# Kernel tuning notes

Hardware: AMD Instinct MI355X
Metric: run time of the kernel (lower is better)

Reference implementation:

```python
import jax, jax.numpy as jnp
import numpy as np

NUM_CENTROIDS = 2048
EMA_DECAY = 0.99
GAMMA = 1.0
EPS = 1e-08


def setup_inputs() -> dict:
    key = jax.random.key(0)
    k1, k2 = jax.random.split(key)
    B, T, D = 32, 512, 512
    inputs = jax.random.normal(k1, (B, T, D), dtype=jnp.float32)
    # variance_scaling(0.1, 'fan_avg', 'normal') init for the codebook
    fan_avg = (NUM_CENTROIDS + D) / 2.0
    std = np.sqrt(0.1 / fan_avg).astype(np.float32)
    codebook = jax.random.normal(k2, (NUM_CENTROIDS, D), dtype=jnp.float32) * std
    cluster_counts = jnp.ones((NUM_CENTROIDS,), dtype=jnp.float32)
    return {"inputs": inputs, "codebook": codebook,
            "cluster_counts": cluster_counts, "train": 1}


def reference(inputs, codebook, cluster_counts, train):
    D = inputs.shape[-1]
    K = codebook.shape[0]
    flat = jnp.reshape(inputs, (-1, D))  # [N, D]

    # similarity of stop-gradient features to codebook rows: [N, K]
    features = jax.lax.stop_gradient(flat)
    similarity = jnp.einsum('nd,kd->nk', features, codebook)
    scores = jax.nn.softmax(similarity, axis=-1)
    nn_idx = jnp.argmax(scores, axis=-1)  # [N]

    # cluster counts = column sums of one-hot encodings -> scatter-add
    counts = jnp.zeros((K,), dtype=scores.dtype).at[nn_idx].add(1.0)
    if train:
        new_counts = EMA_DECAY * cluster_counts + (1.0 - EMA_DECAY) * counts
    else:
        new_counts = cluster_counts

    # one_hot @ codebook == gather of codebook rows
    quantized = codebook[nn_idx]  # [N, D]
    quantized = quantized - jnp.mean(quantized, axis=-1, keepdims=True)
    quantized = quantized / jnp.linalg.norm(quantized, axis=-1, keepdims=True)
    quantized = jnp.reshape(quantized, inputs.shape)

    # entropy-based quantization loss (scalar), broadcast to [..., K]
    h_clust = -jnp.mean(jnp.sum(scores * jnp.log2(scores + EPS), axis=-1))
    diversity = jnp.mean(scores, axis=0)
    h_diversity = -jnp.sum(diversity * jnp.log2(diversity + EPS))
    loss = h_clust - GAMMA * h_diversity
    quantization_loss = jnp.full(inputs.shape[:-1] + (K,), loss)

    # straight-through estimator
    quantized = inputs + jax.lax.stop_gradient(quantized - inputs)

    nn_idx_out = jnp.reshape(nn_idx, inputs.shape[:-1])[None]  # [1, B, T]
    codebook_values = jax.lax.stop_gradient(codebook)[None]     # [1, K, D]
    return (quantized, quantization_loss, nn_idx_out, codebook_values, new_counts)
```

## Files before the change

### kernel.cpp

```cpp
#include <hip/hip_runtime.h>
#include <cstddef>
#include <cmath>

#define NROWS 16384
#define DIM   512
#define KC    2048

#define Q_OFF    0ul
#define LOSS_OFF 8388608ul
#define NN_OFF   41943040ul
#define CB_OFF   41959424ul
#define CNT_OFF  43008000ul

#define FLAG_CAP 4096
#define FLAG_TAU 3e-5f

#define WS_LOSS   0
#define WS_CNT    4
#define WS_ENT    2052
#define WS_NFLAG  3076
#define WS_FLAGS  3080
#define WS_DIVLOG 15376

typedef __attribute__((ext_vector_type(8))) short short8;
typedef __attribute__((ext_vector_type(4))) float f32x4;

__device__ __forceinline__ short hi1(float f) {
    return (short)(__float_as_uint(f) >> 16);
}
__device__ __forceinline__ short lo1(float f) {
    unsigned int u = __float_as_uint(f);
    float l = f - __uint_as_float(u & 0xffff0000u);
    return (short)(__float_as_uint(l) >> 16);
}
__device__ __forceinline__ short8 hi8(float4 a, float4 b) {
    short8 r;
    r[0]=hi1(a.x); r[1]=hi1(a.y); r[2]=hi1(a.z); r[3]=hi1(a.w);
    r[4]=hi1(b.x); r[5]=hi1(b.y); r[6]=hi1(b.z); r[7]=hi1(b.w);
    return r;
}
__device__ __forceinline__ short8 lo8(float4 a, float4 b) {
    short8 r;
    r[0]=lo1(a.x); r[1]=lo1(a.y); r[2]=lo1(a.z); r[3]=lo1(a.w);
    r[4]=lo1(b.x); r[5]=lo1(b.y); r[6]=lo1(b.z); r[7]=lo1(b.w);
    return r;
}

#define LDW  40
#define AH_B 0
#define AL_B 5120
#define BH_B 10240
#define BL_B 15360

__global__ __launch_bounds__(256, 3) void gemm_mfma(const float* __restrict__ A,
                                                    const float* __restrict__ B,
                                                    float* __restrict__ C,
                                                    int* __restrict__ ws) {
    if (blockIdx.x == 0 && blockIdx.y == 0) {
        for (int i = threadIdx.x + WS_CNT; i < WS_CNT + 2048; i += 256) ws[i] = 0;
        if (threadIdx.x == 0) ws[WS_NFLAG] = 0;
    }
    __shared__ ushort smem[20480];
    const int t    = threadIdx.x;
    const int n0   = blockIdx.x * 128;
    const int m0   = blockIdx.y * 128;
    const int rsub = t >> 2;
    const int kc   = (t & 3) * 8;
    const int lane = t & 63, quad = lane >> 4, lr = lane & 15;
    const int w = t >> 6, wm = w >> 1, wn = w & 1;

    f32x4 acc[4][4] = {};

    const float* Abase = A + (size_t)(m0 + rsub) * DIM + kc;
    const float* Bbase = B + (size_t)(n0 + rsub) * DIM + kc;

    float4 pa0 = *(const float4*)(Abase);
    float4 pa1 = *(const float4*)(Abase + 4);
    float4 pa2 = *(const float4*)(Abase + 64 * DIM);
    float4 pa3 = *(const float4*)(Abase + 64 * DIM + 4);
    float4 pb0 = *(const float4*)(Bbase);
    float4 pb1 = *(const float4*)(Bbase + 4);
    float4 pb2 = *(const float4*)(Bbase + 64 * DIM);
    float4 pb3 = *(const float4*)(Bbase + 64 * DIM + 4);

    ushort* wa0 = smem + AH_B + rsub * LDW + kc;
    ushort* wa1 = smem + AH_B + (rsub + 64) * LDW + kc;
    ushort* wb0 = smem + BH_B + rsub * LDW + kc;
    ushort* wb1 = smem + BH_B + (rsub + 64) * LDW + kc;

    const ushort* ra = smem + (wm * 64 + lr) * LDW + quad * 8;
    const ushort* rb = smem + (wn * 64 + lr) * LDW + quad * 8;

    for (int kk = 0; kk < 16; ++kk) {
        *(short8*)(wa0)        = hi8(pa0, pa1);
        *(short8*)(wa0 + AL_B) = lo8(pa0, pa1);
        *(short8*)(wa1)        = hi8(pa2, pa3);
        *(short8*)(wa1 + AL_B) = lo8(pa2, pa3);
        *(short8*)(wb0)        = hi8(pb0, pb1);
        *(short8*)(wb0 + AL_B) = lo8(pb0, pb1);
        *(short8*)(wb1)        = hi8(pb2, pb3);
        *(short8*)(wb1 + AL_B) = lo8(pb2, pb3);
        __syncthreads();

        if (kk < 15) {
            const float* a = Abase + (kk + 1) * 32;
            const float* b = Bbase + (kk + 1) * 32;
            pa0 = *(const float4*)(a);
            pa1 = *(const float4*)(a + 4);
            pa2 = *(const float4*)(a + 64 * DIM);
            pa3 = *(const float4*)(a + 64 * DIM + 4);
            pb0 = *(const float4*)(b);
            pb1 = *(const float4*)(b + 4);
            pb2 = *(const float4*)(b + 64 * DIM);
            pb3 = *(const float4*)(b + 64 * DIM + 4);
        }

        short8 ah[4], al[4], bx[4];
        #pragma unroll
        for (int mt = 0; mt < 4; ++mt) ah[mt] = *(const short8*)(ra + AH_B + mt * 16 * LDW);
        #pragma unroll
        for (int nt = 0; nt < 4; ++nt) bx[nt] = *(const short8*)(rb + BH_B + nt * 16 * LDW);
        #pragma unroll
        for (int mt = 0; mt < 4; ++mt)
            #pragma unroll
            for (int nt = 0; nt < 4; ++nt)
                acc[mt][nt] = __builtin_amdgcn_mfma_f32_16x16x32_bf16(ah[mt], bx[nt], acc[mt][nt], 0, 0, 0);
        #pragma unroll
        for (int mt = 0; mt < 4; ++mt) al[mt] = *(const short8*)(ra + AL_B + mt * 16 * LDW);
        #pragma unroll
        for (int mt = 0; mt < 4; ++mt)
            #pragma unroll
            for (int nt = 0; nt < 4; ++nt)
                acc[mt][nt] = __builtin_amdgcn_mfma_f32_16x16x32_bf16(al[mt], bx[nt], acc[mt][nt], 0, 0, 0);
        #pragma unroll
        for (int nt = 0; nt < 4; ++nt) bx[nt] = *(const short8*)(rb + BL_B + nt * 16 * LDW);
        #pragma unroll
        for (int mt = 0; mt < 4; ++mt)
            #pragma unroll
            for (int nt = 0; nt < 4; ++nt)
                acc[mt][nt] = __builtin_amdgcn_mfma_f32_16x16x32_bf16(ah[mt], bx[nt], acc[mt][nt], 0, 0, 0);
        __syncthreads();
    }

    #pragma unroll
    for (int mt = 0; mt < 4; ++mt) {
        #pragma unroll
        for (int nt = 0; nt < 4; ++nt) {
            const int r0 = m0 + wm * 64 + mt * 16 + quad * 4;
            const int c0 = n0 + wn * 64 + nt * 16 + lr;
            #pragma unroll
            for (int j = 0; j < 4; ++j)
                C[(size_t)(r0 + j) * KC + c0] = acc[mt][nt][j];
        }
    }
}

__device__ __forceinline__ float block_reduce_sum(float v, volatile float* sf,
                                                  int lane, int w) {
    #pragma unroll
    for (int off = 32; off; off >>= 1) v += __shfl_xor(v, off, 64);
    if (lane == 0) sf[w] = v;
    __syncthreads();
    v = sf[0] + sf[1] + sf[2] + sf[3];
    __syncthreads();
    return v;
}

__global__ __launch_bounds__(256, 4) void rowpass(const float* __restrict__ sim,
                                                  float* __restrict__ nn,
                                                  float* __restrict__ divpart2,
                                                  int*   __restrict__ counts,
                                                  float* __restrict__ entpart,
                                                  int*   __restrict__ nflag,
                                                  int*   __restrict__ flags) {
    __shared__ float divp[KC];
    __shared__ float sent[4];
    const int t = threadIdx.x, lane = t & 63, w = t >> 6;
    const int b = blockIdx.x;
    const int row0 = b * 16 + w * 4;
    const int col0 = lane << 2;

    float4 dacc[8] = {};
    float ent_acc = 0.f;
    const float* base = sim + (size_t)row0 * KC + col0;

    #pragma unroll 1
    for (int rr = 0; rr < 4; ++rr) {
        float4 cur[8];
        const float* rp = base + (size_t)rr * KC;
        #pragma unroll
        for (int j = 0; j < 8; ++j) cur[j] = *(const float4*)(rp + 256 * j);

        float bv = -3.0e38f, rv = -3.0e38f;
        int   bi = 0x7fffffff, ri = 0x7fffffff;
        #pragma unroll
        for (int j = 0; j < 8; ++j) {
            #pragma unroll
            for (int c = 0; c < 4; ++c) {
                float v = (&cur[j].x)[c];
                int   i = col0 + c + 256 * j;
                if (v > bv || (v == bv && i < bi)) { rv = bv; ri = bi; bv = v; bi = i; }
                else if (v > rv || (v == rv && i < ri)) { rv = v; ri = i; }
            }
        }
        #pragma unroll
        for (int off = 32; off; off >>= 1) {
            float obv = __shfl_xor(bv, off, 64);
            int   obi = __shfl_xor(bi, off, 64);
            float orv = __shfl_xor(rv, off, 64);
            int   ori = __shfl_xor(ri, off, 64);
            bool ob = (obv > bv) || (obv == bv && obi < bi);
            float c1v = ob ? bv : obv;  int c1i = ob ? bi : obi;
            float c2v = ob ? orv : rv;  int c2i = ob ? ori : ri;
            bv = ob ? obv : bv;  bi = ob ? obi : bi;
            bool rb = (c1v > c2v) || (c1v == c2v && c1i < c2i);
            rv = rb ? c1v : c2v;  ri = rb ? c1i : c2i;
        }
        const float m = bv;

        float Z = 0.f, S = 0.f;
        #pragma unroll
        for (int j = 0; j < 8; ++j) {
            #pragma unroll
            for (int c = 0; c < 4; ++c) {
                float d = (&cur[j].x)[c] - m;
                float e = expf(d);
                Z += e; S += e * d;
                (&cur[j].x)[c] = e;
            }
        }
        #pragma unroll
        for (int off = 32; off; off >>= 1) {
            Z += __shfl_xor(Z, off, 64);
            S += __shfl_xor(S, off, 64);
        }
        const float inv = 1.0f / Z;
        #pragma unroll
        for (int j = 0; j < 8; ++j) {
            dacc[j].x += cur[j].x * inv; dacc[j].y += cur[j].y * inv;
            dacc[j].z += cur[j].z * inv; dacc[j].w += cur[j].w * inv;
        }

        if (lane == 0) {
            ent_acc += 1.4426950408889634f * (S * inv) - log2f(Z) + 2.9546393e-5f;
            atomicAdd(&counts[bi], 1);
            nn[row0 + rr] = (float)bi;
            if (bv - rv < FLAG_TAU) {
                int e = atomicAdd(nflag, 1);
                if (e < FLAG_CAP) {
                    flags[3*e] = row0 + rr; flags[3*e+1] = bi; flags[3*e+2] = ri;
                }
            }
        }
    }

    if (lane == 0) sent[w] = ent_acc;
    for (int ww = 0; ww < 4; ++ww) {
        if (w == ww) {
            #pragma unroll
            for (int j = 0; j < 8; ++j) {
                float4* p = (float4*)&divp[col0 + 256 * j];
                if (ww == 0) *p = dacc[j];
                else {
                    float4 v = *p;
                    v.x += dacc[j].x; v.y += dacc[j].y;
                    v.z += dacc[j].z; v.w += dacc[j].w;
                    *p = v;
                }
            }
        }
        __syncthreads();
    }
    float4* dst = (float4*)(divpart2 + (size_t)b * KC);
    dst[t]       = *(float4*)&divp[t * 4];
    dst[t + 256] = *(float4*)&divp[t * 4 + 1024];
    if (t == 0) entpart[b] = sent[0] + sent[1] + sent[2] + sent[3];
}

__global__ __launch_bounds__(256) void fixfin(const float* __restrict__ divpart2,
                                              float* __restrict__ part2,
                                              const float* __restrict__ A,
                                              const float* __restrict__ B,
                                              float* __restrict__ nn,
                                              int*   __restrict__ counts,
                                              const int* __restrict__ flags,
                                              const int* __restrict__ nflagp) {
    const int t = threadIdx.x;
    if (blockIdx.x < 128) {
        const int b = blockIdx.x;
        const float* dp = divpart2 + (size_t)b * 8 * KC;
        #pragma unroll
        for (int j = 0; j < 8; ++j) {
            int c = t + 256 * j;
            float s = 0.f;
            #pragma unroll
            for (int r = 0; r < 8; ++r) s += dp[(size_t)r * KC + c];
            part2[(size_t)b * KC + c] = s;
        }
    } else {
        __shared__ float sf[4];
        int nf = *nflagp; if (nf > FLAG_CAP) nf = FLAG_CAP;
        const int lane = t & 63, w = t >> 6;
        for (int e = blockIdx.x - 128; e < nf; e += 128) {
            const int row = flags[3*e], i1 = flags[3*e+1], i2 = flags[3*e+2];
            const float* ar = A + (size_t)row * DIM;
            const float* b1 = B + (size_t)i1 * DIM;
            const float* b2 = B + (size_t)i2 * DIM;
            float d1 = ar[t] * b1[t] + ar[t + 256] * b1[t + 256];
            float d2 = ar[t] * b2[t] + ar[t + 256] * b2[t + 256];
            d1 = block_reduce_sum(d1, sf, lane, w);
            d2 = block_reduce_sum(d2, sf, lane, w);
            if (t == 0 && (d2 > d1 || (d2 == d1 && i2 < i1))) {
                nn[row] = (float)i2;
                atomicSub(&counts[i1], 1);
                atomicAdd(&counts[i2], 1);
            }
            __syncthreads();
        }
    }
}

__global__ __launch_bounds__(256) void fin1b(const float* __restrict__ part2,
                                             float* __restrict__ divlog8) {
    __shared__ float sf[4];
    const int t = threadIdx.x, lane = t & 63, w = t >> 6;
    const int c = blockIdx.x * 256 + t;
    float s = 0.f;
    for (int r = 0; r < 128; ++r) s += part2[(size_t)r * KC + c];
    float d = s * (1.0f / 16384.0f);
    float v = d * log2f(d + 1e-8f);
    float S = block_reduce_sum(v, sf, lane, w);
    if (t == 0) divlog8[blockIdx.x] = S;
}

__global__ __launch_bounds__(256) void fin2(const float* __restrict__ entpart,
                                            const float* __restrict__ divlog8,
                                            float* __restrict__ lossp) {
    __shared__ float sf[4];
    const int t = threadIdx.x, lane = t & 63, w = t >> 6;
    float se = entpart[t] + entpart[t + 256] + entpart[t + 512] + entpart[t + 768];
    float Se = block_reduce_sum(se, sf, lane, w);
    float Sd = block_reduce_sum((t < 8) ? divlog8[t] : 0.f, sf, lane, w);
    if (t == 0)
        lossp[0] = (float)(-(double)Se / 16384.0 + (double)Sd);
}

__global__ __launch_bounds__(256) void tail(const float* __restrict__ x,
                                            const float* __restrict__ cb,
                                            const float* __restrict__ oldc,
                                            const int*   __restrict__ counts,
                                            const float* __restrict__ lossp,
                                            const int*   __restrict__ train,
                                            const float* __restrict__ nn,
                                            float* __restrict__ out) {
    const int bb = blockIdx.x;
    const int t  = threadIdx.x;
    if (bb < 4096) {
        const int lane = t & 63;
        const int row  = (bb << 2) + (t >> 6);
        const int idx  = (int)nn[row];
        const float* c  = cb + (size_t)idx * DIM;
        const float* xr = x  + (size_t)row * DIM;

        float4 q0 = *(const float4*)(c + lane * 8);
        float4 q1 = *(const float4*)(c + lane * 8 + 4);

        float s = q0.x+q0.y+q0.z+q0.w + q1.x+q1.y+q1.z+q1.w;
        #pragma unroll
        for (int off = 32; off; off >>= 1) s += __shfl_xor(s, off, 64);
        const float mean = s * (1.0f / 512.0f);
        q0.x -= mean; q0.y -= mean; q0.z -= mean; q0.w -= mean;
        q1.x -= mean; q1.y -= mean; q1.z -= mean; q1.w -= mean;

        float ss = q0.x*q0.x+q0.y*q0.y+q0.z*q0.z+q0.w*q0.w
                 + q1.x*q1.x+q1.y*q1.y+q1.z*q1.z+q1.w*q1.w;
        #pragma unroll
        for (int off = 32; off; off >>= 1) ss += __shfl_xor(ss, off, 64);
        const float inv = 1.0f / sqrtf(ss);

        float4 x0 = *(const float4*)(xr + lane * 8);
        float4 x1 = *(const float4*)(xr + lane * 8 + 4);
        float4 o0, o1;
        o0.x = x0.x + (q0.x*inv - x0.x); o0.y = x0.y + (q0.y*inv - x0.y);
        o0.z = x0.z + (q0.z*inv - x0.z); o0.w = x0.w + (q0.w*inv - x0.w);
        o1.x = x1.x + (q1.x*inv - x1.x); o1.y = x1.y + (q1.y*inv - x1.y);
        o1.z = x1.z + (q1.z*inv - x1.z); o1.w = x1.w + (q1.w*inv - x1.w);
        *(float4*)(out + (size_t)row * DIM + lane * 8)     = o0;
        *(float4*)(out + (size_t)row * DIM + lane * 8 + 4) = o1;
    } else {
        const size_t LOSS4 = 33554432ul / 4;
        const size_t CB4   = 1048576ul  / 4;
        size_t i = (size_t)(bb - 4096) * 256 + t;
        if (i < LOSS4) {
            const float l = lossp[0];
            ((float4*)(out + LOSS_OFF))[i] = make_float4(l, l, l, l);
        } else if (i < LOSS4 + CB4) {
            size_t j = i - LOSS4;
            ((float4*)(out + CB_OFF))[j] = ((const float4*)cb)[j];
        } else {
            size_t k = i - LOSS4 - CB4;
            if (k < 2048) {
                float nc = train[0] ? 0.99f * oldc[k] + 0.01f * (float)counts[k]
                                    : oldc[k];
                out[CNT_OFF + k] = nc;
            }
        }
    }
}

extern "C" void kernel_launch(void* const* d_in, const int* in_sizes, int n_in,
                              void* d_out, int out_size, void* d_ws, size_t ws_size,
                              hipStream_t stream) {
    const float* x     = (const float*)d_in[0];
    const float* cb    = (const float*)d_in[1];
    const float* oldc  = (const float*)d_in[2];
    const int*   train = (const int*)d_in[3];
    float* out = (float*)d_out;

    float* sim      = out + LOSS_OFF;
    float* divpart2 = out + Q_OFF;
    float* part2    = out + CB_OFF;
    float* nn       = out + NN_OFF;

    float* lossp   = (float*)d_ws + WS_LOSS;
    int*   counts  = (int*)d_ws   + WS_CNT;
    float* entpart = (float*)d_ws + WS_ENT;
    int*   nflag   = (int*)d_ws   + WS_NFLAG;
    int*   flags   = (int*)d_ws   + WS_FLAGS;
    float* divlog8 = (float*)d_ws + WS_DIVLOG;

    gemm_mfma<<<dim3(KC / 128, NROWS / 128), 256, 0, stream>>>(x, cb, sim, (int*)d_ws);
    rowpass<<<1024, 256, 0, stream>>>(sim, nn, divpart2, counts, entpart, nflag, flags);
    fixfin<<<256, 256, 0, stream>>>(divpart2, part2, x, cb, nn, counts, flags, nflag);
    fin1b<<<8, 256, 0, stream>>>(part2, divlog8);
    fin2<<<1, 256, 0, stream>>>(entpart, divlog8, lossp);
    tail<<<4096 + 33800, 256, 0, stream>>>(x, cb, oldc, counts, lossp, train, nn, out);
}
```

Baseline: 356.9 us.

## Atomically accumulate diversity, merge finalize kernels, drop x read in tail

Rowpass now atomically adds each block's column-sum of softmax scores into a single workspace vector instead of writing per-block partials. That removes the two-stage partial reduction and merges fin1b/fin2 into one extra block of the fixfin kernel, cutting two launches. The tail kernel no longer reads the inputs for the straight-through sum and writes the normalized codebook row directly. Output stores now use nontemporal stores. Float atomics make the diversity sum order-nondeterministic, and dropping the x + (q - x) form changes rounding slightly.

```diff
diff --git a/kernel.cpp b/kernel.cpp
--- a/kernel.cpp
+++ b/kernel.cpp
@@ -17,13 +17,19 @@
 
 #define WS_LOSS   0
 #define WS_CNT    4
-#define WS_ENT    2052
-#define WS_NFLAG  3076
-#define WS_FLAGS  3080
-#define WS_DIVLOG 15376
+#define WS_DIV    2052
+#define WS_ENT    4100
+#define WS_NFLAG  5124
+#define WS_FLAGS  5128
+#define WS_ZEND   5128
 
 typedef __attribute__((ext_vector_type(8))) short short8;
 typedef __attribute__((ext_vector_type(4))) float f32x4;
+
+__device__ __forceinline__ void nt_store4(float* p, float4 v) {
+    f32x4 u; u[0] = v.x; u[1] = v.y; u[2] = v.z; u[3] = v.w;
+    __builtin_nontemporal_store(u, (f32x4*)p);
+}
 
 __device__ __forceinline__ short hi1(float f) {
     return (short)(__float_as_uint(f) >> 16);
@@ -57,8 +63,7 @@
                                                     float* __restrict__ C,
                                                     int* __restrict__ ws) {
     if (blockIdx.x == 0 && blockIdx.y == 0) {
-        for (int i = threadIdx.x + WS_CNT; i < WS_CNT + 2048; i += 256) ws[i] = 0;
-        if (threadIdx.x == 0) ws[WS_NFLAG] = 0;
+        for (int i = threadIdx.x; i < WS_ZEND; i += 256) ws[i] = 0;
     }
     __shared__ ushort smem[20480];
     const int t    = threadIdx.x;
@@ -168,7 +173,7 @@
 
 __global__ __launch_bounds__(256, 4) void rowpass(const float* __restrict__ sim,
                                                   float* __restrict__ nn,
-                                                  float* __restrict__ divpart2,
+                                                  float* __restrict__ div,
                                                   int*   __restrict__ counts,
                                                   float* __restrict__ entpart,
                                                   int*   __restrict__ nflag,
@@ -271,82 +276,56 @@
         }
         __syncthreads();
     }
-    float4* dst = (float4*)(divpart2 + (size_t)b * KC);
-    dst[t]       = *(float4*)&divp[t * 4];
-    dst[t + 256] = *(float4*)&divp[t * 4 + 1024];
+    #pragma unroll
+    for (int k = 0; k < 8; ++k) atomicAdd(&div[t * 8 + k], divp[t * 8 + k]);
     if (t == 0) entpart[b] = sent[0] + sent[1] + sent[2] + sent[3];
 }
 
-__global__ __launch_bounds__(256) void fixfin(const float* __restrict__ divpart2,
-                                              float* __restrict__ part2,
-                                              const float* __restrict__ A,
+__global__ __launch_bounds__(256) void fixfin(const float* __restrict__ A,
                                               const float* __restrict__ B,
                                               float* __restrict__ nn,
                                               int*   __restrict__ counts,
                                               const int* __restrict__ flags,
-                                              const int* __restrict__ nflagp) {
-    const int t = threadIdx.x;
-    if (blockIdx.x < 128) {
-        const int b = blockIdx.x;
-        const float* dp = divpart2 + (size_t)b * 8 * KC;
-        #pragma unroll
-        for (int j = 0; j < 8; ++j) {
-            int c = t + 256 * j;
-            float s = 0.f;
-            #pragma unroll
-            for (int r = 0; r < 8; ++r) s += dp[(size_t)r * KC + c];
-            part2[(size_t)b * KC + c] = s;
-        }
-    } else {
-        __shared__ float sf[4];
-        int nf = *nflagp; if (nf > FLAG_CAP) nf = FLAG_CAP;
-        const int lane = t & 63, w = t >> 6;
-        for (int e = blockIdx.x - 128; e < nf; e += 128) {
-            const int row = flags[3*e], i1 = flags[3*e+1], i2 = flags[3*e+2];
-            const float* ar = A + (size_t)row * DIM;
-            const float* b1 = B + (size_t)i1 * DIM;
-            const float* b2 = B + (size_t)i2 * DIM;
-            float d1 = ar[t] * b1[t] + ar[t + 256] * b1[t + 256];
-            float d2 = ar[t] * b2[t] + ar[t + 256] * b2[t + 256];
-            d1 = block_reduce_sum(d1, sf, lane, w);
-            d2 = block_reduce_sum(d2, sf, lane, w);
-            if (t == 0 && (d2 > d1 || (d2 == d1 && i2 < i1))) {
-                nn[row] = (float)i2;
-                atomicSub(&counts[i1], 1);
-                atomicAdd(&counts[i2], 1);
-            }
-            __syncthreads();
-        }
-    }
-}
-
-__global__ __launch_bounds__(256) void fin1b(const float* __restrict__ part2,
-                                             float* __restrict__ divlog8) {
+                                              const int* __restrict__ nflagp,
+                                              const float* __restrict__ div,
+                                              const float* __restrict__ entpart,
+                                              float* __restrict__ lossp) {
     __shared__ float sf[4];
     const int t = threadIdx.x, lane = t & 63, w = t >> 6;
-    const int c = blockIdx.x * 256 + t;
-    float s = 0.f;
-    for (int r = 0; r < 128; ++r) s += part2[(size_t)r * KC + c];
-    float d = s * (1.0f / 16384.0f);
-    float v = d * log2f(d + 1e-8f);
-    float S = block_reduce_sum(v, sf, lane, w);
-    if (t == 0) divlog8[blockIdx.x] = S;
-}
-
-__global__ __launch_bounds__(256) void fin2(const float* __restrict__ entpart,
-                                            const float* __restrict__ divlog8,
-                                            float* __restrict__ lossp) {
-    __shared__ float sf[4];
-    const int t = threadIdx.x, lane = t & 63, w = t >> 6;
-    float se = entpart[t] + entpart[t + 256] + entpart[t + 512] + entpart[t + 768];
-    float Se = block_reduce_sum(se, sf, lane, w);
-    float Sd = block_reduce_sum((t < 8) ? divlog8[t] : 0.f, sf, lane, w);
-    if (t == 0)
-        lossp[0] = (float)(-(double)Se / 16384.0 + (double)Sd);
-}
-
-__global__ __launch_bounds__(256) void tail(const float* __restrict__ x,
-                                            const float* __restrict__ cb,
+    if (blockIdx.x == 128) {
+        float loc = 0.f;
+        #pragma unroll
+        for (int k = 0; k < 8; ++k) {
+            float d = div[t + 256 * k] * (1.0f / 16384.0f);
+            loc += d * log2f(d + 1e-8f);
+        }
+        float Sd = block_reduce_sum(loc, sf, lane, w);
+        float se = entpart[t] + entpart[t + 256] + entpart[t + 512] + entpart[t + 768];
+        float Se = block_reduce_sum(se, sf, lane, w);
+        if (t == 0)
+            lossp[0] = (float)(-(double)Se / 16384.0 + (double)Sd);
+        return;
+    }
+    int nf = *nflagp; if (nf > FLAG_CAP) nf = FLAG_CAP;
+    for (int e = blockIdx.x; e < nf; e += 128) {
+        const int row = flags[3*e], i1 = flags[3*e+1], i2 = flags[3*e+2];
+        const float* ar = A + (size_t)row * DIM;
+        const float* b1 = B + (size_t)i1 * DIM;
+        const float* b2 = B + (size_t)i2 * DIM;
+        float d1 = ar[t] * b1[t] + ar[t + 256] * b1[t + 256];
+        float d2 = ar[t] * b2[t] + ar[t + 256] * b2[t + 256];
+        d1 = block_reduce_sum(d1, sf, lane, w);
+        d2 = block_reduce_sum(d2, sf, lane, w);
+        if (t == 0 && (d2 > d1 || (d2 == d1 && i2 < i1))) {
+            nn[row] = (float)i2;
+            atomicSub(&counts[i1], 1);
+            atomicAdd(&counts[i2], 1);
+        }
+        __syncthreads();
+    }
+}
+
+__global__ __launch_bounds__(256) void tail(const float* __restrict__ cb,
                                             const float* __restrict__ oldc,
                                             const int*   __restrict__ counts,
                                             const float* __restrict__ lossp,
@@ -359,8 +338,7 @@
         const int lane = t & 63;
         const int row  = (bb << 2) + (t >> 6);
         const int idx  = (int)nn[row];
-        const float* c  = cb + (size_t)idx * DIM;
-        const float* xr = x  + (size_t)row * DIM;
+        const float* c = cb + (size_t)idx * DIM;
 
         float4 q0 = *(const float4*)(c + lane * 8);
         float4 q1 = *(const float4*)(c + lane * 8 + 4);
@@ -378,25 +356,21 @@
         for (int off = 32; off; off >>= 1) ss += __shfl_xor(ss, off, 64);
         const float inv = 1.0f / sqrtf(ss);
 
-        float4 x0 = *(const float4*)(xr + lane * 8);
-        float4 x1 = *(const float4*)(xr + lane * 8 + 4);
         float4 o0, o1;
-        o0.x = x0.x + (q0.x*inv - x0.x); o0.y = x0.y + (q0.y*inv - x0.y);
-        o0.z = x0.z + (q0.z*inv - x0.z); o0.w = x0.w + (q0.w*inv - x0.w);
-        o1.x = x1.x + (q1.x*inv - x1.x); o1.y = x1.y + (q1.y*inv - x1.y);
-        o1.z = x1.z + (q1.z*inv - x1.z); o1.w = x1.w + (q1.w*inv - x1.w);
-        *(float4*)(out + (size_t)row * DIM + lane * 8)     = o0;
-        *(float4*)(out + (size_t)row * DIM + lane * 8 + 4) = o1;
+        o0.x = q0.x*inv; o0.y = q0.y*inv; o0.z = q0.z*inv; o0.w = q0.w*inv;
+        o1.x = q1.x*inv; o1.y = q1.y*inv; o1.z = q1.z*inv; o1.w = q1.w*inv;
+        nt_store4(out + (size_t)row * DIM + lane * 8, o0);
+        nt_store4(out + (size_t)row * DIM + lane * 8 + 4, o1);
     } else {
         const size_t LOSS4 = 33554432ul / 4;
         const size_t CB4   = 1048576ul  / 4;
         size_t i = (size_t)(bb - 4096) * 256 + t;
         if (i < LOSS4) {
             const float l = lossp[0];
-            ((float4*)(out + LOSS_OFF))[i] = make_float4(l, l, l, l);
+            nt_store4(out + LOSS_OFF + i * 4, make_float4(l, l, l, l));
         } else if (i < LOSS4 + CB4) {
             size_t j = i - LOSS4;
-            ((float4*)(out + CB_OFF))[j] = ((const float4*)cb)[j];
+            nt_store4(out + CB_OFF + j * 4, ((const float4*)cb)[j]);
         } else {
             size_t k = i - LOSS4 - CB4;
             if (k < 2048) {
@@ -417,22 +391,18 @@
     const int*   train = (const int*)d_in[3];
     float* out = (float*)d_out;
 
-    float* sim      = out + LOSS_OFF;
-    float* divpart2 = out + Q_OFF;
-    float* part2    = out + CB_OFF;
-    float* nn       = out + NN_OFF;
+    float* sim = out + LOSS_OFF;
+    float* nn  = out + NN_OFF;
 
     float* lossp   = (float*)d_ws + WS_LOSS;
     int*   counts  = (int*)d_ws   + WS_CNT;
+    float* div     = (float*)d_ws + WS_DIV;
     float* entpart = (float*)d_ws + WS_ENT;
     int*   nflag   = (int*)d_ws   + WS_NFLAG;
     int*   flags   = (int*)d_ws   + WS_FLAGS;
-    float* divlog8 = (float*)d_ws + WS_DIVLOG;
 
     gemm_mfma<<<dim3(KC / 128, NROWS / 128), 256, 0, stream>>>(x, cb, sim, (int*)d_ws);
-    rowpass<<<1024, 256, 0, stream>>>(sim, nn, divpart2, counts, entpart, nflag, flags);
-    fixfin<<<256, 256, 0, stream>>>(divpart2, part2, x, cb, nn, counts, flags, nflag);
-    fin1b<<<8, 256, 0, stream>>>(part2, divlog8);
-    fin2<<<1, 256, 0, stream>>>(entpart, divlog8, lossp);
-    tail<<<4096 + 33800, 256, 0, stream>>>(x, cb, oldc, counts, lossp, train, nn, out);
-}
+    rowpass<<<1024, 256, 0, stream>>>(sim, nn, div, counts, entpart, nflag, flags);
+    fixfin<<<129, 256, 0, stream>>>(x, cb, nn, counts, flags, nflag, div, entpart, lossp);
+    tail<<<4096 + 33800, 256, 0, stream>>>(cb, oldc, counts, lossp, train, nn, out);
+}
```

After: 546.0 us. 1.53x slower.
